# Kernel optimization log

Hardware: AMD Instinct MI355X
Metric: run time of the kernel (lower is better)

Reference implementation:

```python
import jax, jax.numpy as jnp
import numpy as np

TWO_PI = 2.0 * np.pi
POW25_7 = 25.0 ** 7
M_RGB2XYZ = np.array([[0.4124564, 0.3575761, 0.1804375],
                      [0.2126729, 0.7151522, 0.072175],
                      [0.0193339, 0.119192, 0.9503041]], dtype=np.float32)
XYZ_REF = np.array([0.95047, 1.0, 1.08883], dtype=np.float32)


def rgb_to_lab(rgb):
    # rgb: [B, 3] in [0, 1]
    lin = jnp.where(rgb > 0.04045, ((rgb + 0.055) / 1.055) ** 2.4, rgb / 12.92)
    xyz = lin @ jnp.asarray(M_RGB2XYZ).T
    xyz_n = xyz / jnp.asarray(XYZ_REF)
    f = jnp.where(xyz_n > 0.008856, jnp.cbrt(xyz_n), 7.787 * xyz_n + 16.0 / 116.0)
    L = 116.0 * f[:, 1] - 16.0
    a = 500.0 * (f[:, 0] - f[:, 1])
    b = 200.0 * (f[:, 1] - f[:, 2])
    return L, a, b


def delta_e_2000(lab1, lab2):
    L1, a1, b1 = lab1
    L2, a2, b2 = lab2
    C1 = jnp.sqrt(a1 ** 2 + b1 ** 2)
    C2 = jnp.sqrt(a2 ** 2 + b2 ** 2)
    C_avg = (C1 + C2) / 2
    C_avg7 = C_avg ** 7
    G = 0.5 * (1 - jnp.sqrt(C_avg7 / (C_avg7 + POW25_7)))
    a1p = a1 * (1 + G)
    a2p = a2 * (1 + G)
    C1p = jnp.sqrt(a1p ** 2 + b1 ** 2)
    C2p = jnp.sqrt(a2p ** 2 + b2 ** 2)
    h1p = jnp.arctan2(b1, a1p) % TWO_PI
    h2p = jnp.arctan2(b2, a2p) % TWO_PI
    dL = L2 - L1
    dC = C2p - C1p
    dh = h2p - h1p
    dh = jnp.where(jnp.abs(dh) > np.pi,
                   jnp.where(h2p <= h1p, dh + TWO_PI, dh - TWO_PI), dh)
    dH = 2 * jnp.sqrt(C1p * C2p) * jnp.sin(dh / 2)
    L_avg = (L1 + L2) / 2
    Cp_avg = (C1p + C2p) / 2
    h_avg = jnp.where(jnp.abs(h1p - h2p) > np.pi,
                      (h1p + h2p + TWO_PI) / 2, (h1p + h2p) / 2)
    T = (1 - 0.17 * jnp.cos(h_avg - np.pi / 6)
         + 0.24 * jnp.cos(2 * h_avg)
         + 0.32 * jnp.cos(3 * h_avg + np.pi / 30)
         - 0.2 * jnp.cos(4 * h_avg - 7 * np.pi / 20))
    theta = 30 * jnp.exp(-(((h_avg * 180.0 / np.pi) - 275.0) / 25.0) ** 2)
    Cp_avg7 = Cp_avg ** 7
    RC = 2 * jnp.sqrt(Cp_avg7 / (Cp_avg7 + POW25_7))
    RT = -jnp.sin(2 * theta) * RC
    SL = 1 + 0.015 * (L_avg - 50) ** 2 / jnp.sqrt(20 + (L_avg - 50) ** 2)
    SC = 1 + 0.045 * Cp_avg
    SH = 1 + 0.015 * Cp_avg * T
    return jnp.sqrt((dL / SL) ** 2 + (dC / SC) ** 2 + (dH / SH) ** 2
                    + RT * (dC / SC) * (dH / SH))


def setup_inputs() -> dict:
    key = jax.random.key(0)
    k1, k2 = jax.random.split(key)
    B = 16777216
    pred = jax.random.uniform(k1, (B, 3), dtype=jnp.float32)
    target = jax.random.uniform(k2, (B, 3), dtype=jnp.float32)
    return {"pred": pred, "target": target}


def reference(pred, target):
    mse_loss = jnp.mean((pred - target) ** 2, axis=1)  # [B]
    de = delta_e_2000(rgb_to_lab(pred), rgb_to_lab(target))  # [B]
    # original detaches delta_e (computed on CPU numpy, written into a new tensor)
    combined = 0.2 * mse_loss + 0.8 * jax.lax.stop_gradient(de)
    return jnp.mean(combined)
```

## Files before the change

kernel.cpp:

```cpp
#include <hip/hip_runtime.h>
#include <math.h>

#define TPB 256
#define MAXBLOCKS 8192

__device__ __forceinline__ float fsqrt_(float x){ return __builtin_amdgcn_sqrtf(x); }
__device__ __forceinline__ float frcp_ (float x){ return __builtin_amdgcn_rcpf(x); }
__device__ __forceinline__ float frsq_ (float x){ return __builtin_amdgcn_rsqf(x); }
__device__ __forceinline__ float fpow_(float x, float y){ return __expf(y * __logf(x)); }

__device__ __forceinline__ float srgb_lin(float c){
    float p = fpow_((c + 0.055f) * (1.0f/1.055f), 2.4f);
    return (c > 0.04045f) ? p : c * (1.0f/12.92f);
}
__device__ __forceinline__ float lab_f(float t){
    float cb = fpow_(t, 1.0f/3.0f);
    return (t > 0.008856f) ? cb : fmaf(7.787f, t, 16.0f/116.0f);
}

__device__ __forceinline__ void rgb2lab(float r, float g, float b,
                                        float& L, float& A, float& Bv){
    float lr = srgb_lin(r), lg = srgb_lin(g), lb = srgb_lin(b);
    float xn = fmaf(0.4124564f, lr, fmaf(0.3575761f, lg, 0.1804375f*lb)) * (1.0f/0.95047f);
    float yn = fmaf(0.2126729f, lr, fmaf(0.7151522f, lg, 0.072175f *lb));
    float zn = fmaf(0.0193339f, lr, fmaf(0.119192f , lg, 0.9503041f*lb)) * (1.0f/1.08883f);
    float fx = lab_f(xn), fy = lab_f(yn), fz = lab_f(zn);
    L  = fmaf(116.0f, fy, -16.0f);
    A  = 500.0f * (fx - fy);
    Bv = 200.0f * (fy - fz);
}

__device__ __forceinline__ float fast_atan2_2pi(float y, float x){
    float ax = fabsf(x), ay = fabsf(y);
    float mx = fmaxf(ax, ay), mn = fminf(ax, ay);
    float t = mn * frcp_(fmaxf(mx, 1e-38f));
    float s = t * t;
    float p = -0.01172120f;
    p = fmaf(p, s,  0.05265332f);
    p = fmaf(p, s, -0.11643287f);
    p = fmaf(p, s,  0.19354346f);
    p = fmaf(p, s, -0.33262347f);
    p = fmaf(p, s,  0.99997726f);
    p = p * t;
    float r = (ay > ax) ? (1.57079632679f - p) : p;
    r = (x < 0.0f) ? (3.14159265359f - r) : r;
    r = (y < 0.0f) ? (6.28318530718f - r) : r;
    return r;
}

__device__ __forceinline__ float row_loss(float pr, float pg, float pb,
                                          float tr, float tg, float tb){
    const float PI_   = 3.14159265359f;
    const float T2PI  = 6.28318530718f;
    const float P257  = 6103515625.0f;

    float dr = pr - tr, dg = pg - tg, db = pb - tb;
    float mse = (dr*dr + dg*dg + db*db) * (1.0f/3.0f);

    float L1, a1, b1, L2, a2, b2;
    rgb2lab(pr, pg, pb, L1, a1, b1);
    rgb2lab(tr, tg, tb, L2, a2, b2);

    float C1 = fsqrt_(fmaf(a1, a1, b1*b1));
    float C2 = fsqrt_(fmaf(a2, a2, b2*b2));
    float Cav = 0.5f * (C1 + C2);
    float c2 = Cav*Cav;
    float c7 = c2*c2*c2*Cav;
    float G = 0.5f * (1.0f - fsqrt_(c7 * frcp_(c7 + P257)));
    float a1p = a1 * (1.0f + G);
    float a2p = a2 * (1.0f + G);
    float C1p = fsqrt_(fmaf(a1p, a1p, b1*b1));
    float C2p = fsqrt_(fmaf(a2p, a2p, b2*b2));
    float h1p = fast_atan2_2pi(b1, a1p);
    float h2p = fast_atan2_2pi(b2, a2p);

    float dL = L2 - L1;
    float dC = C2p - C1p;
    float dh = h2p - h1p;
    if (fabsf(dh) > PI_) dh = (h2p <= h1p) ? (dh + T2PI) : (dh - T2PI);
    float dH = 2.0f * fsqrt_(C1p * C2p) * __sinf(0.5f * dh);

    float Lav  = 0.5f * (L1 + L2);
    float Cpav = 0.5f * (C1p + C2p);
    float hsum = h1p + h2p;
    float hav = (fabsf(h1p - h2p) > PI_) ? 0.5f*(hsum + T2PI) : 0.5f*hsum;

    float T = 1.0f
            - 0.17f * __cosf(hav - 0.52359877559f)
            + 0.24f * __cosf(2.0f * hav)
            + 0.32f * __cosf(fmaf(3.0f, hav,  0.10471975512f))
            - 0.20f * __cosf(fmaf(4.0f, hav, -1.09955742876f));

    float u = fmaf(hav, 57.2957795131f, -275.0f) * 0.04f;
    float theta = 30.0f * __expf(-u*u);

    float cp2 = Cpav*Cpav;
    float cp7 = cp2*cp2*cp2*Cpav;
    float RC = 2.0f * fsqrt_(cp7 * frcp_(cp7 + P257));
    float RT = -__sinf(2.0f * theta) * RC;

    float Lm = Lav - 50.0f;
    float Lm2 = Lm * Lm;
    float SL = fmaf(0.015f * Lm2, frsq_(20.0f + Lm2), 1.0f);
    float SC = fmaf(0.045f, Cpav, 1.0f);
    float SH = fmaf(0.015f * Cpav, T, 1.0f);

    float t1 = dL * frcp_(SL);
    float t2 = dC * frcp_(SC);
    float t3 = dH * frcp_(SH);
    float arg = fmaf(t1, t1, fmaf(t2, t2, fmaf(t3, t3, RT*t2*t3)));
    float de = fsqrt_(fmaxf(arg, 0.0f));

    return fmaf(0.2f, mse, 0.8f * de);
}

__global__ void __launch_bounds__(TPB)
de_main(const float* __restrict__ pred, const float* __restrict__ tgt,
        float* __restrict__ partials, int B){
    int nvec = B >> 2;
    int gid = blockIdx.x * TPB + threadIdx.x;
    int stride = gridDim.x * TPB;
    float acc = 0.0f;

    for (int i = gid; i < nvec; i += stride){
        const float4* p4 = (const float4*)pred + (size_t)i * 3;
        const float4* t4 = (const float4*)tgt  + (size_t)i * 3;
        float4 pA = p4[0], pB = p4[1], pC = p4[2];
        float4 tA = t4[0], tB = t4[1], tC = t4[2];
        acc += row_loss(pA.x, pA.y, pA.z, tA.x, tA.y, tA.z);
        acc += row_loss(pA.w, pB.x, pB.y, tA.w, tB.x, tB.y);
        acc += row_loss(pB.z, pB.w, pC.x, tB.z, tB.w, tC.x);
        acc += row_loss(pC.y, pC.z, pC.w, tC.y, tC.z, tC.w);
    }
    int r = (nvec << 2) + gid;
    if (r < B){
        acc += row_loss(pred[(size_t)r*3], pred[(size_t)r*3+1], pred[(size_t)r*3+2],
                        tgt [(size_t)r*3], tgt [(size_t)r*3+1], tgt [(size_t)r*3+2]);
    }

    __shared__ float sdata[TPB];
    sdata[threadIdx.x] = acc;
    __syncthreads();
    #pragma unroll
    for (int s = TPB/2; s > 0; s >>= 1){
        if (threadIdx.x < s) sdata[threadIdx.x] += sdata[threadIdx.x + s];
        __syncthreads();
    }
    if (threadIdx.x == 0) partials[blockIdx.x] = sdata[0];
}

__global__ void __launch_bounds__(TPB)
de_final(const float* __restrict__ partials, int n, float* __restrict__ out, double invB){
    __shared__ double sd[TPB];
    double acc = 0.0;
    for (int i = threadIdx.x; i < n; i += TPB) acc += (double)partials[i];
    sd[threadIdx.x] = acc;
    __syncthreads();
    #pragma unroll
    for (int s = TPB/2; s > 0; s >>= 1){
        if (threadIdx.x < s) sd[threadIdx.x] += sd[threadIdx.x + s];
        __syncthreads();
    }
    if (threadIdx.x == 0) out[0] = (float)(sd[0] * invB);
}

extern "C" void kernel_launch(void* const* d_in, const int* in_sizes, int n_in,
                              void* d_out, int out_size, void* d_ws, size_t ws_size,
                              hipStream_t stream){
    const float* pred = (const float*)d_in[0];
    const float* tgt  = (const float*)d_in[1];
    int B = in_sizes[0] / 3;

    int nvec = B >> 2;
    int blocks = (nvec + TPB - 1) / TPB;
    if (blocks > MAXBLOCKS) blocks = MAXBLOCKS;
    size_t wcap = ws_size / sizeof(float);
    if (wcap > 0 && (size_t)blocks > wcap) blocks = (int)wcap;
    if (blocks < 1) blocks = 1;

    float* partials = (float*)d_ws;
    de_main <<<blocks, TPB, 0, stream>>>(pred, tgt, partials, B);
    de_final<<<1, TPB, 0, stream>>>(partials, blocks, (float*)d_out, 1.0/(double)B);
}
```

Measured before the change: 452.4 us.

## Replace hue angle trig with vector algebra in CIEDE2000 kernel

Computes dH straight from dot and cross products of the a'/b' vectors, with no per-pair atan2 and no sin. The mean hue comes from one atan2 of the chroma-weighted sum vector, and the T cosine terms are expanded into multiple-angle polynomials in cos and sin of that mean hue. pow and exp now use native log2 and exp2 builtins. This removes two atan2 calls and several transcendental evaluations per row, in exchange for more FMAs and possible small numerical differences at edge cases such as zero chroma.

```diff
diff --git a/kernel.cpp b/kernel.cpp
--- a/kernel.cpp
+++ b/kernel.cpp
@@ -7,7 +7,9 @@
 __device__ __forceinline__ float fsqrt_(float x){ return __builtin_amdgcn_sqrtf(x); }
 __device__ __forceinline__ float frcp_ (float x){ return __builtin_amdgcn_rcpf(x); }
 __device__ __forceinline__ float frsq_ (float x){ return __builtin_amdgcn_rsqf(x); }
-__device__ __forceinline__ float fpow_(float x, float y){ return __expf(y * __logf(x)); }
+__device__ __forceinline__ float flog2_(float x){ return __builtin_amdgcn_logf(x); }
+__device__ __forceinline__ float fexp2_(float x){ return __builtin_amdgcn_exp2f(x); }
+__device__ __forceinline__ float fpow_(float x, float y){ return fexp2_(y * flog2_(x)); }
 
 __device__ __forceinline__ float srgb_lin(float c){
     float p = fpow_((c + 0.055f) * (1.0f/1.055f), 2.4f);
@@ -50,9 +52,7 @@
 
 __device__ __forceinline__ float row_loss(float pr, float pg, float pb,
                                           float tr, float tg, float tb){
-    const float PI_   = 3.14159265359f;
-    const float T2PI  = 6.28318530718f;
-    const float P257  = 6103515625.0f;
+    const float P257 = 6103515625.0f;
 
     float dr = pr - tr, dg = pg - tg, db = pb - tb;
     float mse = (dr*dr + dg*dg + db*db) * (1.0f/3.0f);
@@ -64,35 +64,49 @@
     float C1 = fsqrt_(fmaf(a1, a1, b1*b1));
     float C2 = fsqrt_(fmaf(a2, a2, b2*b2));
     float Cav = 0.5f * (C1 + C2);
-    float c2 = Cav*Cav;
-    float c7 = c2*c2*c2*Cav;
-    float G = 0.5f * (1.0f - fsqrt_(c7 * frcp_(c7 + P257)));
-    float a1p = a1 * (1.0f + G);
-    float a2p = a2 * (1.0f + G);
+    float c2v = Cav*Cav;
+    float c7 = c2v*c2v*c2v*Cav;
+    float gs = fsqrt_(c7 * frcp_(c7 + P257));
+    float opG = fmaf(-0.5f, gs, 1.5f);
+    float a1p = a1 * opG;
+    float a2p = a2 * opG;
     float C1p = fsqrt_(fmaf(a1p, a1p, b1*b1));
     float C2p = fsqrt_(fmaf(a2p, a2p, b2*b2));
-    float h1p = fast_atan2_2pi(b1, a1p);
-    float h2p = fast_atan2_2pi(b2, a2p);
 
     float dL = L2 - L1;
     float dC = C2p - C1p;
-    float dh = h2p - h1p;
-    if (fabsf(dh) > PI_) dh = (h2p <= h1p) ? (dh + T2PI) : (dh - T2PI);
-    float dH = 2.0f * fsqrt_(C1p * C2p) * __sinf(0.5f * dh);
+
+    float prod  = C1p * C2p;
+    float dot   = fmaf(a1p, a2p, b1*b2);
+    float cross = fmaf(a1p, b2, -(a2p*b1));
+    float dH = copysignf(fsqrt_(fmaxf(2.0f*(prod - dot), 0.0f)), cross);
 
     float Lav  = 0.5f * (L1 + L2);
     float Cpav = 0.5f * (C1p + C2p);
-    float hsum = h1p + h2p;
-    float hav = (fabsf(h1p - h2p) > PI_) ? 0.5f*(hsum + T2PI) : 0.5f*hsum;
 
-    float T = 1.0f
-            - 0.17f * __cosf(hav - 0.52359877559f)
-            + 0.24f * __cosf(2.0f * hav)
-            + 0.32f * __cosf(fmaf(3.0f, hav,  0.10471975512f))
-            - 0.20f * __cosf(fmaf(4.0f, hav, -1.09955742876f));
+    float vx = fmaf(a1p, C2p, a2p*C1p);
+    float vy = fmaf(b1 , C2p, b2 *C1p);
+    float hav = fast_atan2_2pi(vy, vx);
+    float inv = frsq_(fmaxf(fmaf(vx, vx, vy*vy), 1e-30f));
+    float ch = vx * inv, sh = vy * inv;
 
-    float u = fmaf(hav, 57.2957795131f, -275.0f) * 0.04f;
-    float theta = 30.0f * __expf(-u*u);
+    float cos2 = fmaf(2.0f*ch, ch, -1.0f);
+    float sin2 = 2.0f * sh * ch;
+    float cos3 = ch * fmaf(2.0f, cos2, -1.0f);
+    float sin3 = sh * fmaf(2.0f, cos2,  1.0f);
+    float cos4 = fmaf(2.0f*cos2, cos2, -1.0f);
+    float sin4 = 2.0f * sin2 * cos2;
+    float T = 1.0f;
+    T = fmaf(-0.147224319f, ch,   T);
+    T = fmaf(-0.085f,       sh,   T);
+    T = fmaf( 0.24f,        cos2, T);
+    T = fmaf( 0.318247006f, cos3, T);
+    T = fmaf(-0.033449109f, sin3, T);
+    T = fmaf(-0.090798100f, cos4, T);
+    T = fmaf(-0.178201305f, sin4, T);
+
+    float u = fmaf(hav, 2.29183118f, -11.0f);
+    float theta = 30.0f * fexp2_(-1.44269504f * (u*u));
 
     float cp2 = Cpav*Cpav;
     float cp7 = cp2*cp2*cp2*Cpav;
```

Measured after the change: 428.0 us. -5.4%, faster.

## Vectorize row loss over four rows and replace trig with algebraic identities

Applied to the files above, without the earlier changes.

Processes four rows at once as ext_vector_type(4) values and switches to raw amdgcn log2/exp2/sin intrinsics. The hue difference term is now computed from dot and cross products instead of two atan2 calls plus a sine. The hue mean comes from one atan2 of a summed vector, and the cosine series for T uses multiple-angle identities instead of four cosines. The reference-white division is folded into the matrix constants. This removes many transcendental ops in a compute-bound kernel, at the cost of small numeric differences and possible register-pressure increase from the four-wide code.

```diff
diff --git a/kernel.cpp b/kernel.cpp
--- a/kernel.cpp
+++ b/kernel.cpp
@@ -3,115 +3,166 @@
 
 #define TPB 256
 #define MAXBLOCKS 8192
+
+typedef float v4f __attribute__((ext_vector_type(4)));
 
 __device__ __forceinline__ float fsqrt_(float x){ return __builtin_amdgcn_sqrtf(x); }
 __device__ __forceinline__ float frcp_ (float x){ return __builtin_amdgcn_rcpf(x); }
 __device__ __forceinline__ float frsq_ (float x){ return __builtin_amdgcn_rsqf(x); }
-__device__ __forceinline__ float fpow_(float x, float y){ return __expf(y * __logf(x)); }
-
-__device__ __forceinline__ float srgb_lin(float c){
-    float p = fpow_((c + 0.055f) * (1.0f/1.055f), 2.4f);
-    return (c > 0.04045f) ? p : c * (1.0f/12.92f);
-}
-__device__ __forceinline__ float lab_f(float t){
-    float cb = fpow_(t, 1.0f/3.0f);
-    return (t > 0.008856f) ? cb : fmaf(7.787f, t, 16.0f/116.0f);
-}
-
-__device__ __forceinline__ void rgb2lab(float r, float g, float b,
-                                        float& L, float& A, float& Bv){
-    float lr = srgb_lin(r), lg = srgb_lin(g), lb = srgb_lin(b);
-    float xn = fmaf(0.4124564f, lr, fmaf(0.3575761f, lg, 0.1804375f*lb)) * (1.0f/0.95047f);
-    float yn = fmaf(0.2126729f, lr, fmaf(0.7151522f, lg, 0.072175f *lb));
-    float zn = fmaf(0.0193339f, lr, fmaf(0.119192f , lg, 0.9503041f*lb)) * (1.0f/1.08883f);
-    float fx = lab_f(xn), fy = lab_f(yn), fz = lab_f(zn);
-    L  = fmaf(116.0f, fy, -16.0f);
-    A  = 500.0f * (fx - fy);
-    Bv = 200.0f * (fy - fz);
-}
-
-__device__ __forceinline__ float fast_atan2_2pi(float y, float x){
-    float ax = fabsf(x), ay = fabsf(y);
-    float mx = fmaxf(ax, ay), mn = fminf(ax, ay);
-    float t = mn * frcp_(fmaxf(mx, 1e-38f));
-    float s = t * t;
-    float p = -0.01172120f;
-    p = fmaf(p, s,  0.05265332f);
-    p = fmaf(p, s, -0.11643287f);
-    p = fmaf(p, s,  0.19354346f);
-    p = fmaf(p, s, -0.33262347f);
-    p = fmaf(p, s,  0.99997726f);
+__device__ __forceinline__ float flog2_(float x){ return __builtin_amdgcn_logf(x); }
+__device__ __forceinline__ float fexp2_(float x){ return __builtin_amdgcn_exp2f(x); }
+__device__ __forceinline__ float fsinr_(float x){ return __builtin_amdgcn_sinf(x); }
+
+__device__ __forceinline__ v4f vs(float x){ return (v4f){x, x, x, x}; }
+
+#define V4APPLY(fn, a) ((v4f){ fn((a).x), fn((a).y), fn((a).z), fn((a).w) })
+__device__ __forceinline__ v4f vsqrt(v4f a){ return V4APPLY(fsqrt_, a); }
+__device__ __forceinline__ v4f vrcp (v4f a){ return V4APPLY(frcp_ , a); }
+__device__ __forceinline__ v4f vrsq (v4f a){ return V4APPLY(frsq_ , a); }
+__device__ __forceinline__ v4f vlog2(v4f a){ return V4APPLY(flog2_, a); }
+__device__ __forceinline__ v4f vexp2(v4f a){ return V4APPLY(fexp2_, a); }
+__device__ __forceinline__ v4f vsinr(v4f a){ return V4APPLY(fsinr_, a); }
+
+#if __has_builtin(__builtin_elementwise_fma)
+__device__ __forceinline__ v4f vfma(v4f a, v4f b, v4f c){ return __builtin_elementwise_fma(a,b,c); }
+#else
+__device__ __forceinline__ v4f vfma(v4f a, v4f b, v4f c){ return a*b + c; }
+#endif
+__device__ __forceinline__ v4f vmax(v4f a, v4f b){ return __builtin_elementwise_max(a,b); }
+__device__ __forceinline__ v4f vmin(v4f a, v4f b){ return __builtin_elementwise_min(a,b); }
+__device__ __forceinline__ v4f vabs(v4f a){ return __builtin_elementwise_abs(a); }
+__device__ __forceinline__ v4f vselgt(v4f x, float t, v4f a, v4f b){
+    v4f r;
+    r.x = x.x > t ? a.x : b.x;
+    r.y = x.y > t ? a.y : b.y;
+    r.z = x.z > t ? a.z : b.z;
+    r.w = x.w > t ? a.w : b.w;
+    return r;
+}
+__device__ __forceinline__ v4f vcopysign(v4f m, v4f s){
+    v4f r;
+    r.x = copysignf(m.x, s.x);
+    r.y = copysignf(m.y, s.y);
+    r.z = copysignf(m.z, s.z);
+    r.w = copysignf(m.w, s.w);
+    return r;
+}
+
+__device__ __forceinline__ v4f srgb_lin(v4f c){
+    v4f t = (c + vs(0.055f)) * vs(1.0f/1.055f);
+    v4f p = vexp2(vs(2.4f) * vlog2(t));
+    return vselgt(c, 0.04045f, p, c * vs(1.0f/12.92f));
+}
+__device__ __forceinline__ v4f lab_f(v4f t){
+    v4f cb = vexp2(vs(1.0f/3.0f) * vlog2(t));
+    return vselgt(t, 0.008856f, cb, vfma(vs(7.787f), t, vs(16.0f/116.0f)));
+}
+
+__device__ __forceinline__ void rgb2lab(v4f r, v4f g, v4f b, v4f& L, v4f& A, v4f& Bv){
+    v4f lr = srgb_lin(r), lg = srgb_lin(g), lb = srgb_lin(b);
+    v4f xn = vfma(vs(0.4339499f), lr, vfma(vs(0.3762098f), lg, vs(0.1898414f)*lb));
+    v4f yn = vfma(vs(0.2126729f), lr, vfma(vs(0.7151522f), lg, vs(0.0721750f)*lb));
+    v4f zn = vfma(vs(0.0177566f), lr, vfma(vs(0.1094680f), lg, vs(0.8727720f)*lb));
+    v4f fx = lab_f(xn), fy = lab_f(yn), fz = lab_f(zn);
+    L  = vfma(vs(116.0f), fy, vs(-16.0f));
+    A  = vs(500.0f) * (fx - fy);
+    Bv = vs(200.0f) * (fy - fz);
+}
+
+__device__ __forceinline__ v4f vatan2_2pi(v4f y, v4f x){
+    v4f ax = vabs(x), ay = vabs(y);
+    v4f mx = vmax(ax, ay), mn = vmin(ax, ay);
+    v4f t = mn * vrcp(vmax(mx, vs(1e-38f)));
+    v4f s = t * t;
+    v4f p = vs(-0.01172120f);
+    p = vfma(p, s, vs( 0.05265332f));
+    p = vfma(p, s, vs(-0.11643287f));
+    p = vfma(p, s, vs( 0.19354346f));
+    p = vfma(p, s, vs(-0.33262347f));
+    p = vfma(p, s, vs( 0.99997726f));
     p = p * t;
-    float r = (ay > ax) ? (1.57079632679f - p) : p;
-    r = (x < 0.0f) ? (3.14159265359f - r) : r;
-    r = (y < 0.0f) ? (6.28318530718f - r) : r;
+    v4f r = vselgt(ay - ax, 0.0f, vs(1.57079632679f) - p, p);
+    r = vselgt(vs(0.0f) - x, 0.0f, vs(3.14159265359f) - r, r);
+    r = vselgt(vs(0.0f) - y, 0.0f, vs(6.28318530718f) - r, r);
     return r;
 }
 
-__device__ __forceinline__ float row_loss(float pr, float pg, float pb,
-                                          float tr, float tg, float tb){
-    const float PI_   = 3.14159265359f;
-    const float T2PI  = 6.28318530718f;
-    const float P257  = 6103515625.0f;
-
-    float dr = pr - tr, dg = pg - tg, db = pb - tb;
-    float mse = (dr*dr + dg*dg + db*db) * (1.0f/3.0f);
-
-    float L1, a1, b1, L2, a2, b2;
+__device__ __forceinline__ v4f row_loss(v4f pr, v4f pg, v4f pb,
+                                        v4f tr, v4f tg, v4f tb){
+    const float P257 = 6103515625.0f;
+
+    v4f dr = pr - tr, dg = pg - tg, db = pb - tb;
+    v4f mse = (dr*dr + dg*dg + db*db) * vs(1.0f/3.0f);
+
+    v4f L1, a1, b1, L2, a2, b2;
     rgb2lab(pr, pg, pb, L1, a1, b1);
     rgb2lab(tr, tg, tb, L2, a2, b2);
 
-    float C1 = fsqrt_(fmaf(a1, a1, b1*b1));
-    float C2 = fsqrt_(fmaf(a2, a2, b2*b2));
-    float Cav = 0.5f * (C1 + C2);
-    float c2 = Cav*Cav;
-    float c7 = c2*c2*c2*Cav;
-    float G = 0.5f * (1.0f - fsqrt_(c7 * frcp_(c7 + P257)));
-    float a1p = a1 * (1.0f + G);
-    float a2p = a2 * (1.0f + G);
-    float C1p = fsqrt_(fmaf(a1p, a1p, b1*b1));
-    float C2p = fsqrt_(fmaf(a2p, a2p, b2*b2));
-    float h1p = fast_atan2_2pi(b1, a1p);
-    float h2p = fast_atan2_2pi(b2, a2p);
-
-    float dL = L2 - L1;
-    float dC = C2p - C1p;
-    float dh = h2p - h1p;
-    if (fabsf(dh) > PI_) dh = (h2p <= h1p) ? (dh + T2PI) : (dh - T2PI);
-    float dH = 2.0f * fsqrt_(C1p * C2p) * __sinf(0.5f * dh);
-
-    float Lav  = 0.5f * (L1 + L2);
-    float Cpav = 0.5f * (C1p + C2p);
-    float hsum = h1p + h2p;
-    float hav = (fabsf(h1p - h2p) > PI_) ? 0.5f*(hsum + T2PI) : 0.5f*hsum;
-
-    float T = 1.0f
-            - 0.17f * __cosf(hav - 0.52359877559f)
-            + 0.24f * __cosf(2.0f * hav)
-            + 0.32f * __cosf(fmaf(3.0f, hav,  0.10471975512f))
-            - 0.20f * __cosf(fmaf(4.0f, hav, -1.09955742876f));
-
-    float u = fmaf(hav, 57.2957795131f, -275.0f) * 0.04f;
-    float theta = 30.0f * __expf(-u*u);
-
-    float cp2 = Cpav*Cpav;
-    float cp7 = cp2*cp2*cp2*Cpav;
-    float RC = 2.0f * fsqrt_(cp7 * frcp_(cp7 + P257));
-    float RT = -__sinf(2.0f * theta) * RC;
-
-    float Lm = Lav - 50.0f;
-    float Lm2 = Lm * Lm;
-    float SL = fmaf(0.015f * Lm2, frsq_(20.0f + Lm2), 1.0f);
-    float SC = fmaf(0.045f, Cpav, 1.0f);
-    float SH = fmaf(0.015f * Cpav, T, 1.0f);
-
-    float t1 = dL * frcp_(SL);
-    float t2 = dC * frcp_(SC);
-    float t3 = dH * frcp_(SH);
-    float arg = fmaf(t1, t1, fmaf(t2, t2, fmaf(t3, t3, RT*t2*t3)));
-    float de = fsqrt_(fmaxf(arg, 0.0f));
-
-    return fmaf(0.2f, mse, 0.8f * de);
+    v4f C1 = vsqrt(vfma(a1, a1, b1*b1));
+    v4f C2 = vsqrt(vfma(a2, a2, b2*b2));
+    v4f Cav = vs(0.5f) * (C1 + C2);
+    v4f c2v = Cav*Cav;
+    v4f c7 = c2v*c2v*c2v*Cav;
+    v4f gs = vsqrt(c7 * vrcp(c7 + vs(P257)));
+    v4f opG = vfma(vs(-0.5f), gs, vs(1.5f));
+    v4f a1p = a1 * opG;
+    v4f a2p = a2 * opG;
+    v4f C1p = vsqrt(vfma(a1p, a1p, b1*b1));
+    v4f C2p = vsqrt(vfma(a2p, a2p, b2*b2));
+
+    v4f dL = L2 - L1;
+    v4f dC = C2p - C1p;
+
+    v4f prod  = C1p * C2p;
+    v4f dot   = vfma(a1p, a2p, b1*b2);
+    v4f cross = vfma(a1p, b2, vs(0.0f) - a2p*b1);
+    v4f dH = vcopysign(vsqrt(vmax(vs(2.0f)*(prod - dot), vs(0.0f))), cross);
+
+    v4f Lav  = vs(0.5f) * (L1 + L2);
+    v4f Cpav = vs(0.5f) * (C1p + C2p);
+
+    v4f vx = vfma(a1p, C2p, a2p*C1p);
+    v4f vy = vfma(b1 , C2p, b2 *C1p);
+    v4f hav = vatan2_2pi(vy, vx);
+    v4f inv = vrsq(vmax(vfma(vx, vx, vy*vy), vs(1e-30f)));
+    v4f ch = vx * inv, sh = vy * inv;
+
+    v4f cos2 = vfma(vs(2.0f)*ch, ch, vs(-1.0f));
+    v4f sin2 = vs(2.0f) * sh * ch;
+    v4f cos3 = ch * vfma(vs(2.0f), cos2, vs(-1.0f));
+    v4f sin3 = sh * vfma(vs(2.0f), cos2, vs( 1.0f));
+    v4f cos4 = vfma(vs(2.0f)*cos2, cos2, vs(-1.0f));
+    v4f sin4 = vs(2.0f) * sin2 * cos2;
+    v4f T = vs(1.0f);
+    T = vfma(vs(-0.147224319f), ch,   T);
+    T = vfma(vs(-0.085f),       sh,   T);
+    T = vfma(vs( 0.24f),        cos2, T);
+    T = vfma(vs( 0.318247006f), cos3, T);
+    T = vfma(vs(-0.033449109f), sin3, T);
+    T = vfma(vs(-0.090798100f), cos4, T);
+    T = vfma(vs(-0.178201305f), sin4, T);
+
+    v4f u = vfma(hav, vs(2.29183118f), vs(-11.0f));
+    v4f theta = vs(30.0f) * vexp2(vs(-1.44269504f) * (u*u));
+
+    v4f cp2 = Cpav*Cpav;
+    v4f cp7 = cp2*cp2*cp2*Cpav;
+    v4f RC = vs(2.0f) * vsqrt(cp7 * vrcp(cp7 + vs(P257)));
+    v4f RT = vs(0.0f) - vsinr(theta * vs(0.31830988618f)) * RC;
+
+    v4f Lm = Lav - vs(50.0f);
+    v4f Lm2 = Lm * Lm;
+    v4f SL = vfma(vs(0.015f) * Lm2, vrsq(vs(20.0f) + Lm2), vs(1.0f));
+    v4f SC = vfma(vs(0.045f), Cpav, vs(1.0f));
+    v4f SH = vfma(vs(0.015f) * Cpav, T, vs(1.0f));
+
+    v4f t1 = dL * vrcp(SL);
+    v4f t2 = dC * vrcp(SC);
+    v4f t3 = dH * vrcp(SH);
+    v4f arg = vfma(t1, t1, vfma(t2, t2, vfma(t3, t3, RT*t2*t3)));
+    v4f de = vsqrt(vmax(arg, vs(0.0f)));
+
+    return vfma(vs(0.2f), mse, vs(0.8f) * de);
 }
 
 __global__ void __launch_bounds__(TPB)
@@ -120,22 +171,28 @@
     int nvec = B >> 2;
     int gid = blockIdx.x * TPB + threadIdx.x;
     int stride = gridDim.x * TPB;
-    float acc = 0.0f;
+    v4f acc4 = vs(0.0f);
 
     for (int i = gid; i < nvec; i += stride){
         const float4* p4 = (const float4*)pred + (size_t)i * 3;
         const float4* t4 = (const float4*)tgt  + (size_t)i * 3;
         float4 pA = p4[0], pB = p4[1], pC = p4[2];
         float4 tA = t4[0], tB = t4[1], tC = t4[2];
-        acc += row_loss(pA.x, pA.y, pA.z, tA.x, tA.y, tA.z);
-        acc += row_loss(pA.w, pB.x, pB.y, tA.w, tB.x, tB.y);
-        acc += row_loss(pB.z, pB.w, pC.x, tB.z, tB.w, tC.x);
-        acc += row_loss(pC.y, pC.z, pC.w, tC.y, tC.z, tC.w);
-    }
+        v4f pr = (v4f){pA.x, pA.w, pB.z, pC.y};
+        v4f pg = (v4f){pA.y, pB.x, pB.w, pC.z};
+        v4f pb = (v4f){pA.z, pB.y, pC.x, pC.w};
+        v4f qr = (v4f){tA.x, tA.w, tB.z, tC.y};
+        v4f qg = (v4f){tA.y, tB.x, tB.w, tC.z};
+        v4f qb = (v4f){tA.z, tB.y, tC.x, tC.w};
+        acc4 += row_loss(pr, pg, pb, qr, qg, qb);
+    }
+    float acc = acc4.x + acc4.y + acc4.z + acc4.w;
+
     int r = (nvec << 2) + gid;
     if (r < B){
-        acc += row_loss(pred[(size_t)r*3], pred[(size_t)r*3+1], pred[(size_t)r*3+2],
-                        tgt [(size_t)r*3], tgt [(size_t)r*3+1], tgt [(size_t)r*3+2]);
+        v4f pr = vs(pred[(size_t)r*3]), pg = vs(pred[(size_t)r*3+1]), pb = vs(pred[(size_t)r*3+2]);
+        v4f qr = vs(tgt [(size_t)r*3]), qg = vs(tgt [(size_t)r*3+1]), qb = vs(tgt [(size_t)r*3+2]);
+        acc += row_loss(pr, pg, pb, qr, qg, qb).x;
     }
 
     __shared__ float sdata[TPB];
```

Measured after the change: 417.1 us. 1.08x faster.
